# Kernel optimization log

Measured on AMD Instinct MI355X. Metric: run time of the kernel, lower is better.

Reference implementation:

```python
import jax, jax.numpy as jnp
import numpy as np

EMB = 1024
HEADS = 16
HEAD_DIM = EMB // HEADS
B, T = 2, 2048
LN_EPS = 1e-5  # torch nn.LayerNorm default


def _layernorm(x, g, b):
    # LayerNorm over last dim (head_dim), elementwise affine
    mu = jnp.mean(x, axis=-1, keepdims=True)
    var = jnp.mean(jnp.square(x - mu), axis=-1, keepdims=True)
    return (x - mu) * jax.lax.rsqrt(var + LN_EPS) * g + b


def setup_inputs() -> dict:
    key = jax.random.key(0)
    ks = jax.random.split(key, 6)
    sc = 1.0 / np.sqrt(EMB)  # keep linear outputs O(1)
    return {
        "x": jax.random.normal(ks[0], (B, T, EMB), dtype=jnp.float32),
        "Wk": jax.random.normal(ks[1], (EMB, EMB), dtype=jnp.float32) * sc,
        "Wq": jax.random.normal(ks[2], (EMB, EMB), dtype=jnp.float32) * sc,
        "Wv": jax.random.normal(ks[3], (EMB, EMB), dtype=jnp.float32) * sc,
        "Wu": jax.random.normal(ks[4], (EMB, EMB), dtype=jnp.float32) * sc,
        "bu": jnp.zeros((EMB,), dtype=jnp.float32),
        "kln_g": jnp.ones((HEAD_DIM,), dtype=jnp.float32),
        "kln_b": jnp.zeros((HEAD_DIM,), dtype=jnp.float32),
        "qln_g": jnp.ones((HEAD_DIM,), dtype=jnp.float32),
        "qln_b": jnp.zeros((HEAD_DIM,), dtype=jnp.float32),
    }


def reference(x, Wk, Wq, Wv, Wu, bu, kln_g, kln_b, qln_g, qln_b):
    b, t, e = x.shape
    h, s = HEADS, HEAD_DIM
    # torch Linear (no bias): y = x @ W.T
    keys = (x @ Wk.T).reshape(b, t, h, s)
    queries = (x @ Wq.T).reshape(b, t, h, s)
    values = (x @ Wv.T).reshape(b, t, h, s)
    # per-head LayerNorm (kqnorm=True)
    keys = _layernorm(keys, kln_g, kln_b)
    queries = _layernorm(queries, qln_g, qln_b)
    # NOTE: module scales by emb**(-1/4) on each side (net 1/sqrt(emb), not head dim)
    inv4 = e ** (-0.25)
    queries = queries * inv4
    keys = keys * inv4
    # scores: [b, h, t, t]
    dot = jnp.einsum('bqhs,bkhs->bhqk', queries, keys)
    # causal mask: positions k > q set to -inf (mask_diagonal=False -> diag kept)
    causal = jnp.tril(jnp.ones((t, t), dtype=bool))
    dot = jnp.where(causal, dot, -jnp.inf)
    attn = jax.nn.softmax(dot, axis=-1)
    out = jnp.einsum('bhqk,bkhs->bqhs', attn, values).reshape(b, t, h * s)
    return out @ Wu.T + bu
```

## Files before the change

### kernel.cpp

```cpp
#include <hip/hip_runtime.h>
#include <math.h>

#define EMB 1024
#define NHEADS 16
#define HDIM 64
#define BATCH 2
#define SEQ 2048
#define MROWS (BATCH*SEQ)
#define LN_EPS 1e-5f
#define GK 1024
#define GN 1024

typedef __attribute__((ext_vector_type(8))) short bf16x8;
typedef __attribute__((ext_vector_type(4))) short s16x4;
typedef __attribute__((ext_vector_type(4))) float f32x4;
typedef __attribute__((ext_vector_type(16))) float f32x16;
typedef __attribute__((ext_vector_type(4))) int int4v;

__device__ __forceinline__ short f2bf(float f) {
    union { float f; unsigned u; } v; v.f = f;
    unsigned r = v.u + 0x7FFFu + ((v.u >> 16) & 1u);
    return (short)(r >> 16);
}
__device__ __forceinline__ float bf2f(short s) {
    union { unsigned u; float f; } v; v.u = ((unsigned)(unsigned short)s) << 16;
    return v.f;
}
__device__ __forceinline__ unsigned pk2(short a, short b) {
    return (unsigned)(unsigned short)a | ((unsigned)(unsigned short)b << 16);
}
__device__ __forceinline__ float fexp2(float x) {
    return __builtin_amdgcn_exp2f(x);
}

__device__ __forceinline__ void gload16(const short* g, short* l) {
    __builtin_amdgcn_global_load_lds(
        (const __attribute__((address_space(1))) unsigned*)g,
        (__attribute__((address_space(3))) unsigned*)l, 16, 0, 0);
}

#define MFMA32(a, b, c) __builtin_amdgcn_mfma_f32_32x32x16_bf16(a, b, c, 0, 0, 0)

#define SRC_G(r, c)  ((((c) - ((r) >> 1)) & 3) * 8)
#define RD_G(r, l4)  ((((l4) + ((r) >> 1)) & 3) * 8)

__global__ __launch_bounds__(256)
void cvt_all(const float* __restrict__ X, short* __restrict__ XH,
             const float* __restrict__ W0, const float* __restrict__ W1,
             const float* __restrict__ W2, const float* __restrict__ W3,
             short* __restrict__ WH)
{
    const int zy = blockIdx.y;
    if (zy == 0) {
        const size_t i = (size_t)blockIdx.x * 1024 + threadIdx.x * 4;
        const float4 v = *(const float4*)&X[i];
        s16x4 h;
        h[0] = f2bf(v.x); h[1] = f2bf(v.y);
        h[2] = f2bf(v.z); h[3] = f2bf(v.w);
        *(s16x4*)&XH[i] = h;
    } else {
        const int z = zy - 1;
        if (blockIdx.x >= 1024) return;
        const float* W = (z == 0) ? W0 : (z == 1) ? W1 : (z == 2) ? W2 : W3;
        const size_t i = (size_t)blockIdx.x * 1024 + threadIdx.x * 4;
        const float4 v = *(const float4*)&W[i];
        s16x4 h;
        h[0] = f2bf(v.x); h[1] = f2bf(v.y);
        h[2] = f2bf(v.z); h[3] = f2bf(v.w);
        *(s16x4*)&WH[((size_t)z << 20) + i] = h;
    }
}

__global__ __launch_bounds__(256, 3)
void gemm_kqv(const short* __restrict__ Xh, const short* __restrict__ W4h,
              const float* __restrict__ kg, const float* __restrict__ kb,
              const float* __restrict__ qg, const float* __restrict__ qb,
              float scaleK, float scaleQ,
              short* __restrict__ KhP, short* __restrict__ QhP,
              short* __restrict__ VTh)
{
    __shared__ short AhS[3][128][32], BhS[3][128][32];

    const int t   = threadIdx.x;
    const int ln  = t & 63, wv = t >> 6;
    const int l15 = ln & 15, l4 = ln >> 4;
    const int m0  = blockIdx.y * 128;
    const int n0  = blockIdx.x * 128;
    const int z   = blockIdx.z;
    const int wr  = (wv >> 1) * 64, wc = (wv & 1) * 64;

    const short* Bh = W4h + ((size_t)z << 20);

    const short* gplane = (wv < 2) ? Xh : Bh;
    const int    grow0  = (wv < 2) ? m0 : n0;
    short* lbase = (wv < 2) ? &AhS[0][0][0] : &BhS[0][0][0];
    const int s0 = (wv & 1) ? 4 : 0;

    f32x4 acc[4][4];
    #pragma unroll
    for (int i = 0; i < 4; ++i)
        #pragma unroll
        for (int j = 0; j < 4; ++j) acc[i][j] = (f32x4){0.f, 0.f, 0.f, 0.f};

    #pragma unroll
    for (int s = 0; s < 4; ++s) {
        const int chunk = (s0 + s) * 64 + ln;
        const int r = chunk >> 2, c = chunk & 3;
        gload16(gplane + (size_t)(grow0 + r) * GK + SRC_G(r, c),
                lbase + (s0 + s) * 512);
    }
    #pragma unroll
    for (int s = 0; s < 4; ++s) {
        const int chunk = (s0 + s) * 64 + ln;
        const int r = chunk >> 2, c = chunk & 3;
        gload16(gplane + (size_t)(grow0 + r) * GK + 32 + SRC_G(r, c),
                lbase + 4096 + (s0 + s) * 512);
    }
    asm volatile("s_waitcnt vmcnt(4)" ::: "memory");
    __builtin_amdgcn_s_barrier();

    int cur = 0;
    for (int i = 0; i < 32; ++i) {
        const int cur2 = (cur == 0) ? 2 : cur - 1;
        if (i + 2 < 32) {
            short* lp = lbase + cur2 * 4096;
            const int kof = (i + 2) * 32;
            #pragma unroll
            for (int s = 0; s < 4; ++s) {
                const int chunk = (s0 + s) * 64 + ln;
                const int r = chunk >> 2, c = chunk & 3;
                gload16(gplane + (size_t)(grow0 + r) * GK + kof + SRC_G(r, c),
                        lp + (s0 + s) * 512);
            }
        }

        bf16x8 ah[4], bh[4];
        #pragma unroll
        for (int f = 0; f < 4; ++f) {
            const int ra = wr + f * 16 + l15;
            const int rb = wc + f * 16 + l15;
            ah[f] = *(const bf16x8*)&AhS[cur][ra][RD_G(ra, l4)];
            bh[f] = *(const bf16x8*)&BhS[cur][rb][RD_G(rb, l4)];
        }
        #pragma unroll
        for (int i2 = 0; i2 < 4; ++i2)
            #pragma unroll
            for (int j = 0; j < 4; ++j)
                acc[i2][j] = __builtin_amdgcn_mfma_f32_16x16x32_bf16(ah[i2], bh[j], acc[i2][j], 0, 0, 0);

        if (i + 2 < 32) {
            asm volatile("s_waitcnt vmcnt(4)" ::: "memory");
        } else if (i + 1 < 32) {
            asm volatile("s_waitcnt vmcnt(0)" ::: "memory");
        }
        __builtin_amdgcn_s_barrier();
        cur = (cur == 2) ? 0 : cur + 1;
    }

    if (z < 2) {
        const float* gamma = (z == 0) ? kg : qg;
        const float* beta  = (z == 0) ? kb : qb;
        short* OutH = (z == 0) ? KhP : QhP;
        const float scl = (z == 0) ? scaleK : scaleQ;
        const int n_head = (n0 + wc) >> 6;
        float g4[4], b4[4];
        #pragma unroll
        for (int f = 0; f < 4; ++f) {
            g4[f] = gamma[f * 16 + l15];
            b4[f] = beta [f * 16 + l15];
        }
        #pragma unroll
        for (int i = 0; i < 4; ++i)
            #pragma unroll
            for (int j = 0; j < 4; ++j) {
                const float v0 = acc[i][0][j], v1 = acc[i][1][j];
                const float v2 = acc[i][2][j], v3 = acc[i][3][j];
                float s1 = v0 + v1 + v2 + v3;
                float s2 = v0*v0 + v1*v1 + v2*v2 + v3*v3;
                s1 += __shfl_xor(s1, 1); s2 += __shfl_xor(s2, 1);
                s1 += __shfl_xor(s1, 2); s2 += __shfl_xor(s2, 2);
                s1 += __shfl_xor(s1, 4); s2 += __shfl_xor(s2, 4);
                s1 += __shfl_xor(s1, 8); s2 += __shfl_xor(s2, 8);
                const float mu  = s1 * (1.f / 64.f);
                const float var = s2 * (1.f / 64.f) - mu * mu;
                const float rs  = rsqrtf(var + LN_EPS);
                const int m = m0 + wr + i * 16 + l4 * 4 + j;
                const size_t orow =
                    ((size_t)((m >> 11) * NHEADS + n_head) * SEQ + (m & (SEQ - 1))) * HDIM;
                #pragma unroll
                for (int f = 0; f < 4; ++f) {
                    const float y = ((acc[i][f][j] - mu) * rs * g4[f] + b4[f]) * scl;
                    OutH[orow + f * 16 + l15] = f2bf(y);
                }
            }
    } else {
        #pragma unroll
        for (int i = 0; i < 4; ++i)
            #pragma unroll
            for (int f = 0; f < 4; ++f) {
                s16x4 h4;
                #pragma unroll
                for (int j = 0; j < 4; ++j) h4[j] = f2bf(acc[i][f][j]);
                const int n  = n0 + wc + f * 16 + l15;
                const int hh = n >> 6, dd = n & 63;
                const int mb = m0 + wr + i * 16 + l4 * 4;
                const size_t oa =
                    (((size_t)((mb >> 11) * NHEADS + hh)) * HDIM + dd) * SEQ + (mb & (SEQ - 1));
                *(s16x4*)&VTh[oa] = h4;
            }
    }
}

__global__ __launch_bounds__(256, 2)
void gemm_out(const short* __restrict__ Ah, const short* __restrict__ Bh,
              const float* __restrict__ bias, float* __restrict__ OutF)
{
    __shared__ short AhS[2][64][32], BhS[2][128][32];

    const int t   = threadIdx.x;
    const int ln  = t & 63, wv = t >> 6;
    const int l15 = ln & 15, l4 = ln >> 4;
    const int m0  = blockIdx.y * 64;
    const int n0  = blockIdx.x * 128;
    const int wr  = (wv >> 1) * 32, wc = (wv & 1) * 64;

    const short* gplane = (wv == 0) ? Ah : Bh;
    const int    grow0  = (wv == 0) ? m0 : n0;
    const int    s0     = (wv == 2) ? 4 : 0;
    const int    nseg   = (wv < 3) ? 4 : 0;
    const int    bstep  = (wv == 0) ? 2048 : 4096;
    short* lbase = (wv == 0) ? &AhS[0][0][0] : &BhS[0][0][0];

    f32x4 acc[2][4];
    #pragma unroll
    for (int i = 0; i < 2; ++i)
        #pragma unroll
        for (int j = 0; j < 4; ++j) acc[i][j] = (f32x4){0.f, 0.f, 0.f, 0.f};

    for (int s = 0; s < nseg; ++s) {
        const int chunk = (s0 + s) * 64 + ln;
        const int r = chunk >> 2, c = chunk & 3;
        gload16(gplane + (size_t)(grow0 + r) * GK + SRC_G(r, c),
                lbase + (s0 + s) * 512);
    }
    __syncthreads();

    int cur = 0;
    for (int k0 = 0; k0 < GK; k0 += 32) {
        if (k0 + 32 < GK) {
            short* lp = lbase + (cur ^ 1) * bstep;
            for (int s = 0; s < nseg; ++s) {
                const int chunk = (s0 + s) * 64 + ln;
                const int r = chunk >> 2, c = chunk & 3;
                gload16(gplane + (size_t)(grow0 + r) * GK + k0 + 32 + SRC_G(r, c),
                        lp + (s0 + s) * 512);
            }
        }

        bf16x8 ah[2], bh[4];
        #pragma unroll
        for (int f = 0; f < 2; ++f) {
            const int ra = wr + f * 16 + l15;
            ah[f] = *(const bf16x8*)&AhS[cur][ra][RD_G(ra, l4)];
        }
        #pragma unroll
        for (int f = 0; f < 4; ++f) {
            const int rb = wc + f * 16 + l15;
            bh[f] = *(const bf16x8*)&BhS[cur][rb][RD_G(rb, l4)];
        }
        #pragma unroll
        for (int i = 0; i < 2; ++i)
            #pragma unroll
            for (int j = 0; j < 4; ++j)
                acc[i][j] = __builtin_amdgcn_mfma_f32_16x16x32_bf16(ah[i], bh[j], acc[i][j], 0, 0, 0);

        __syncthreads();
        cur ^= 1;
    }

    float b4[4];
    #pragma unroll
    for (int f = 0; f < 4; ++f) b4[f] = bias[n0 + wc + f * 16 + l15];
    #pragma unroll
    for (int i = 0; i < 2; ++i)
        #pragma unroll
        for (int j = 0; j < 4; ++j) {
            const int m = m0 + wr + i * 16 + l4 * 4 + j;
            const size_t row = (size_t)m * GN + n0 + wc;
            #pragma unroll
            for (int f = 0; f < 4; ++f)
                OutF[row + f * 16 + l15] = acc[i][f][j] + b4[f];
        }
}

__global__ __launch_bounds__(256, 2)
void attn_mfma(const short* __restrict__ Qh, const short* __restrict__ Kh,
               const short* __restrict__ Vh, short* __restrict__ Oh)
{
    __shared__ short KhS[64][64];
    __shared__ short VhS[64][64];

    const int t    = threadIdx.x;
    const int lane = t & 63, wv = t >> 6;
    const int l31  = lane & 31, hb = lane >> 5;
    const int bh   = blockIdx.y;
    const int bb   = bh >> 4, hh = bh & 15;
    const int qt   = bb ? (int)blockIdx.x
                        : (int)gridDim.x - 1 - (int)blockIdx.x;
    const int q0   = qt * 128;
    const int wq0  = wv * 32;

    const size_t kpan = (size_t)bh * SEQ * HDIM;
    const size_t vpan = (size_t)bh * HDIM * SEQ;

    const int sr0  = t >> 3, sr1 = 32 + (t >> 3);
    const int scg  = t & 7;
    const int soff = scg * 8;
    const int lc0  = (scg ^ (sr0 & 7)) * 8;
    const int lc1  = (scg ^ (sr1 & 7)) * 8;

    bf16x8 qfh[4];
    {
        const size_t qrow = kpan + (size_t)(q0 + wq0 + l31) * HDIM;
        #pragma unroll
        for (int ds = 0; ds < 4; ++ds)
            qfh[ds] = *(const bf16x8*)&Qh[qrow + ds * 16 + hb * 8];
    }

    f32x16 oacc0 = (f32x16)(0.0f), oacc1 = (f32x16)(0.0f);
    float m_run = -1e30f, l_run = 0.f;

    const int NT = 2 * qt + 2;

    int4v pKh0, pKh1, pVh0, pVh1;
    {
        pKh0 = *(const int4v*)&Kh[kpan + (size_t)sr0 * HDIM + soff];
        pKh1 = *(const int4v*)&Kh[kpan + (size_t)sr1 * HDIM + soff];
        pVh0 = *(const int4v*)&Vh[vpan + (size_t)sr0 * SEQ + soff];
        pVh1 = *(const int4v*)&Vh[vpan + (size_t)sr1 * SEQ + soff];
    }

    for (int kt = 0; kt < NT; ++kt) {
        const int k0 = kt * 64;

        __syncthreads();

        *(int4v*)&KhS[sr0][lc0] = pKh0;  *(int4v*)&KhS[sr1][lc1] = pKh1;
        *(int4v*)&VhS[sr0][lc0] = pVh0;  *(int4v*)&VhS[sr1][lc1] = pVh1;

        if (kt + 1 < NT) {
            const int kn = k0 + 64;
            pKh0 = *(const int4v*)&Kh[kpan + (size_t)(kn + sr0) * HDIM + soff];
            pKh1 = *(const int4v*)&Kh[kpan + (size_t)(kn + sr1) * HDIM + soff];
            pVh0 = *(const int4v*)&Vh[vpan + (size_t)sr0 * SEQ + kn + soff];
            pVh1 = *(const int4v*)&Vh[vpan + (size_t)sr1 * SEQ + kn + soff];
        }
        __syncthreads();

        if (k0 > q0 + wq0 + 31) continue;

        f32x16 s0 = (f32x16)(0.0f), s1 = (f32x16)(0.0f);
        #pragma unroll
        for (int ds = 0; ds < 4; ++ds) {
            const int g = ((ds * 2 + hb) ^ (l31 & 7)) * 8;
            const bf16x8 kh0 = *(const bf16x8*)&KhS[l31][g];
            const bf16x8 kh1 = *(const bf16x8*)&KhS[32 + l31][g];
            s0 = MFMA32(kh0, qfh[ds], s0);
            s1 = MFMA32(kh1, qfh[ds], s1);
        }

        if (k0 + 63 > q0 + wq0) {
            const int qg = q0 + wq0 + l31;
            #pragma unroll
            for (int reg = 0; reg < 16; ++reg) {
                const int kk = k0 + (reg & 3) + 8 * (reg >> 2) + 4 * hb;
                if (kk > qg)      s0[reg] = -1e30f;
                if (kk + 32 > qg) s1[reg] = -1e30f;
            }
        }

        {
            float mx = -1e30f;
            #pragma unroll
            for (int reg = 0; reg < 16; ++reg)
                mx = fmaxf(mx, fmaxf(s0[reg], s1[reg]));
            mx = fmaxf(mx, __shfl_xor(mx, 32));
            const float mnew = fmaxf(m_run, mx);
            const float scf  = fexp2(m_run - mnew);
            m_run = mnew;
            float ls = 0.f;
            #pragma unroll
            for (int reg = 0; reg < 16; ++reg) {
                const float p0 = fexp2(s0[reg] - mnew);
                const float p1 = fexp2(s1[reg] - mnew);
                s0[reg] = p0; s1[reg] = p1;
                ls += p0 + p1;
            }
            ls += __shfl_xor(ls, 32);
            l_run = l_run * scf + ls;
            #pragma unroll
            for (int reg = 0; reg < 16; ++reg) {
                oacc0[reg] *= scf;
                oacc1[reg] *= scf;
            }
        }

        #pragma unroll
        for (int ks = 0; ks < 4; ++ks) {
            short h8[8];
            #pragma unroll
            for (int a = 0; a < 8; ++a) {
                const float p = (ks >= 2) ? s1[(ks & 1) * 8 + a]
                                          : s0[(ks & 1) * 8 + a];
                h8[a] = f2bf(p);
            }
            const unsigned hA0 = pk2(h8[0], h8[1]), hA1 = pk2(h8[2], h8[3]);
            const unsigned hB0 = pk2(h8[4], h8[5]), hB1 = pk2(h8[6], h8[7]);
            const unsigned hr0 = (unsigned)__shfl_xor((int)(hb ? hA0 : hB0), 32);
            const unsigned hr1 = (unsigned)__shfl_xor((int)(hb ? hA1 : hB1), 32);
            const int4v wih = (int4v){(int)(hb ? hr0 : hA0), (int)(hb ? hr1 : hA1),
                                      (int)(hb ? hB0 : hr0), (int)(hb ? hB1 : hr1)};
            const bf16x8 pfh = __builtin_bit_cast(bf16x8, wih);

            const int gv = ((ks * 2 + hb) ^ (l31 & 7)) * 8;
            const bf16x8 vh0 = *(const bf16x8*)&VhS[l31][gv];
            const bf16x8 vh1 = *(const bf16x8*)&VhS[32 + l31][gv];
            oacc0 = MFMA32(vh0, pfh, oacc0);
            oacc1 = MFMA32(vh1, pfh, oacc1);
        }
    }

    const float inv = 1.f / l_run;
    const int q = q0 + wq0 + l31;
    const size_t row = ((size_t)(bb * SEQ + q)) * EMB + hh * HDIM;
    #pragma unroll
    for (int db = 0; db < 2; ++db)
        #pragma unroll
        for (int b = 0; b < 4; ++b) {
            s16x4 h4;
            #pragma unroll
            for (int a = 0; a < 4; ++a)
                h4[a] = f2bf((db ? oacc1[4 * b + a] : oacc0[4 * b + a]) * inv);
            const int d0 = db * 32 + 8 * b + 4 * hb;
            *(s16x4*)&Oh[row + d0] = h4;
        }
}

extern "C" void kernel_launch(void* const* d_in, const int* in_sizes, int n_in,
                              void* d_out, int out_size, void* d_ws, size_t ws_size,
                              hipStream_t stream)
{
    const float* x  = (const float*)d_in[0];
    const float* Wk = (const float*)d_in[1];
    const float* Wq = (const float*)d_in[2];
    const float* Wv = (const float*)d_in[3];
    const float* Wu = (const float*)d_in[4];
    const float* bu = (const float*)d_in[5];
    const float* kg = (const float*)d_in[6];
    const float* kb = (const float*)d_in[7];
    const float* qg = (const float*)d_in[8];
    const float* qb = (const float*)d_in[9];
    float* out = (float*)d_out;

    char* w = (char*)d_ws;
    short* XhP = (short*)(w);
    short* KhP = (short*)(w + (8u  << 20));
    short* QhP = (short*)(w + (16u << 20));
    short* W4h = (short*)(w + (24u << 20));
    short* VTh = (short*)d_out;

    const float inv4 = 0.17677669529663687f;
    const float l2e  = 1.4426950408889634f;

    cvt_all<<<dim3(4096, 5), 256, 0, stream>>>(x, XhP, Wk, Wq, Wv, Wu, W4h);

    gemm_kqv<<<dim3(GN / 128, MROWS / 128, 3), 256, 0, stream>>>(
        XhP, W4h, kg, kb, qg, qb, inv4, inv4 * l2e,
        KhP, QhP, VTh);

    attn_mfma<<<dim3(SEQ / 128, BATCH * NHEADS), 256, 0, stream>>>(
        QhP, KhP, VTh, XhP);

    gemm_out<<<dim3(GN / 128, MROWS / 64), 256, 0, stream>>>(
        XhP, W4h + (3u << 20), bu, out);
}
```

Before: 121.6 us.

## Stage two K/V tiles per barrier round and skip redundant softmax rescales

```diff
diff --git a/kernel.cpp b/kernel.cpp
--- a/kernel.cpp
+++ b/kernel.cpp
@@ -297,8 +297,8 @@
 void attn_mfma(const short* __restrict__ Qh, const short* __restrict__ Kh,
                const short* __restrict__ Vh, short* __restrict__ Oh)
 {
-    __shared__ short KhS[64][64];
-    __shared__ short VhS[64][64];
+    __shared__ short KhS[2][64][64];
+    __shared__ short VhS[2][64][64];
 
     const int t    = threadIdx.x;
     const int lane = t & 63, wv = t >> 6;
@@ -317,7 +317,6 @@
     const int scg  = t & 7;
     const int soff = scg * 8;
     const int lc0  = (scg ^ (sr0 & 7)) * 8;
-    const int lc1  = (scg ^ (sr1 & 7)) * 8;
 
     bf16x8 qfh[4];
     {
@@ -330,103 +329,121 @@
     f32x16 oacc0 = (f32x16)(0.0f), oacc1 = (f32x16)(0.0f);
     float m_run = -1e30f, l_run = 0.f;
 
-    const int NT = 2 * qt + 2;
-
-    int4v pKh0, pKh1, pVh0, pVh1;
-    {
-        pKh0 = *(const int4v*)&Kh[kpan + (size_t)sr0 * HDIM + soff];
-        pKh1 = *(const int4v*)&Kh[kpan + (size_t)sr1 * HDIM + soff];
-        pVh0 = *(const int4v*)&Vh[vpan + (size_t)sr0 * SEQ + soff];
-        pVh1 = *(const int4v*)&Vh[vpan + (size_t)sr1 * SEQ + soff];
-    }
-
-    for (int kt = 0; kt < NT; ++kt) {
-        const int k0 = kt * 64;
+    const int NR = qt + 1;
+
+    int4v pK[2][2], pV[2][2];
+    #pragma unroll
+    for (int h = 0; h < 2; ++h) {
+        const int kb0 = h * 64;
+        pK[h][0] = *(const int4v*)&Kh[kpan + (size_t)(kb0 + sr0) * HDIM + soff];
+        pK[h][1] = *(const int4v*)&Kh[kpan + (size_t)(kb0 + sr1) * HDIM + soff];
+        pV[h][0] = *(const int4v*)&Vh[vpan + (size_t)sr0 * SEQ + kb0 + soff];
+        pV[h][1] = *(const int4v*)&Vh[vpan + (size_t)sr1 * SEQ + kb0 + soff];
+    }
+
+    for (int rr = 0; rr < NR; ++rr) {
+        const int k0 = rr * 128;
 
         __syncthreads();
 
-        *(int4v*)&KhS[sr0][lc0] = pKh0;  *(int4v*)&KhS[sr1][lc1] = pKh1;
-        *(int4v*)&VhS[sr0][lc0] = pVh0;  *(int4v*)&VhS[sr1][lc1] = pVh1;
-
-        if (kt + 1 < NT) {
-            const int kn = k0 + 64;
-            pKh0 = *(const int4v*)&Kh[kpan + (size_t)(kn + sr0) * HDIM + soff];
-            pKh1 = *(const int4v*)&Kh[kpan + (size_t)(kn + sr1) * HDIM + soff];
-            pVh0 = *(const int4v*)&Vh[vpan + (size_t)sr0 * SEQ + kn + soff];
-            pVh1 = *(const int4v*)&Vh[vpan + (size_t)sr1 * SEQ + kn + soff];
+        #pragma unroll
+        for (int h = 0; h < 2; ++h) {
+            *(int4v*)&KhS[h][sr0][lc0] = pK[h][0];
+            *(int4v*)&KhS[h][sr1][lc0] = pK[h][1];
+            *(int4v*)&VhS[h][sr0][lc0] = pV[h][0];
+            *(int4v*)&VhS[h][sr1][lc0] = pV[h][1];
+        }
+
+        if (rr + 1 < NR) {
+            const int kn = k0 + 128;
+            #pragma unroll
+            for (int h = 0; h < 2; ++h) {
+                const int kb0 = kn + h * 64;
+                pK[h][0] = *(const int4v*)&Kh[kpan + (size_t)(kb0 + sr0) * HDIM + soff];
+                pK[h][1] = *(const int4v*)&Kh[kpan + (size_t)(kb0 + sr1) * HDIM + soff];
+                pV[h][0] = *(const int4v*)&Vh[vpan + (size_t)sr0 * SEQ + kb0 + soff];
+                pV[h][1] = *(const int4v*)&Vh[vpan + (size_t)sr1 * SEQ + kb0 + soff];
+            }
         }
         __syncthreads();
 
-        if (k0 > q0 + wq0 + 31) continue;
-
-        f32x16 s0 = (f32x16)(0.0f), s1 = (f32x16)(0.0f);
-        #pragma unroll
-        for (int ds = 0; ds < 4; ++ds) {
-            const int g = ((ds * 2 + hb) ^ (l31 & 7)) * 8;
-            const bf16x8 kh0 = *(const bf16x8*)&KhS[l31][g];
-            const bf16x8 kh1 = *(const bf16x8*)&KhS[32 + l31][g];
-            s0 = MFMA32(kh0, qfh[ds], s0);
-            s1 = MFMA32(kh1, qfh[ds], s1);
-        }
-
-        if (k0 + 63 > q0 + wq0) {
-            const int qg = q0 + wq0 + l31;
-            #pragma unroll
-            for (int reg = 0; reg < 16; ++reg) {
-                const int kk = k0 + (reg & 3) + 8 * (reg >> 2) + 4 * hb;
-                if (kk > qg)      s0[reg] = -1e30f;
-                if (kk + 32 > qg) s1[reg] = -1e30f;
-            }
-        }
-
-        {
-            float mx = -1e30f;
-            #pragma unroll
-            for (int reg = 0; reg < 16; ++reg)
-                mx = fmaxf(mx, fmaxf(s0[reg], s1[reg]));
-            mx = fmaxf(mx, __shfl_xor(mx, 32));
-            const float mnew = fmaxf(m_run, mx);
-            const float scf  = fexp2(m_run - mnew);
-            m_run = mnew;
-            float ls = 0.f;
-            #pragma unroll
-            for (int reg = 0; reg < 16; ++reg) {
-                const float p0 = fexp2(s0[reg] - mnew);
-                const float p1 = fexp2(s1[reg] - mnew);
-                s0[reg] = p0; s1[reg] = p1;
-                ls += p0 + p1;
-            }
-            ls += __shfl_xor(ls, 32);
-            l_run = l_run * scf + ls;
-            #pragma unroll
-            for (int reg = 0; reg < 16; ++reg) {
-                oacc0[reg] *= scf;
-                oacc1[reg] *= scf;
-            }
-        }
-
-        #pragma unroll
-        for (int ks = 0; ks < 4; ++ks) {
-            short h8[8];
-            #pragma unroll
-            for (int a = 0; a < 8; ++a) {
-                const float p = (ks >= 2) ? s1[(ks & 1) * 8 + a]
-                                          : s0[(ks & 1) * 8 + a];
-                h8[a] = f2bf(p);
-            }
-            const unsigned hA0 = pk2(h8[0], h8[1]), hA1 = pk2(h8[2], h8[3]);
-            const unsigned hB0 = pk2(h8[4], h8[5]), hB1 = pk2(h8[6], h8[7]);
-            const unsigned hr0 = (unsigned)__shfl_xor((int)(hb ? hA0 : hB0), 32);
-            const unsigned hr1 = (unsigned)__shfl_xor((int)(hb ? hA1 : hB1), 32);
-            const int4v wih = (int4v){(int)(hb ? hr0 : hA0), (int)(hb ? hr1 : hA1),
-                                      (int)(hb ? hB0 : hr0), (int)(hb ? hB1 : hr1)};
-            const bf16x8 pfh = __builtin_bit_cast(bf16x8, wih);
-
-            const int gv = ((ks * 2 + hb) ^ (l31 & 7)) * 8;
-            const bf16x8 vh0 = *(const bf16x8*)&VhS[l31][gv];
-            const bf16x8 vh1 = *(const bf16x8*)&VhS[32 + l31][gv];
-            oacc0 = MFMA32(vh0, pfh, oacc0);
-            oacc1 = MFMA32(vh1, pfh, oacc1);
+        #pragma unroll
+        for (int half = 0; half < 2; ++half) {
+            const int kk0 = k0 + half * 64;
+            if (kk0 > q0 + wq0 + 31) continue;
+
+            f32x16 s0 = (f32x16)(0.0f), s1 = (f32x16)(0.0f);
+            #pragma unroll
+            for (int ds = 0; ds < 4; ++ds) {
+                const int g = ((ds * 2 + hb) ^ (l31 & 7)) * 8;
+                const bf16x8 kh0 = *(const bf16x8*)&KhS[half][l31][g];
+                const bf16x8 kh1 = *(const bf16x8*)&KhS[half][32 + l31][g];
+                s0 = MFMA32(kh0, qfh[ds], s0);
+                s1 = MFMA32(kh1, qfh[ds], s1);
+            }
+
+            if (kk0 + 63 > q0 + wq0) {
+                const int qg = q0 + wq0 + l31;
+                #pragma unroll
+                for (int reg = 0; reg < 16; ++reg) {
+                    const int kk = kk0 + (reg & 3) + 8 * (reg >> 2) + 4 * hb;
+                    if (kk > qg)      s0[reg] = -1e30f;
+                    if (kk + 32 > qg) s1[reg] = -1e30f;
+                }
+            }
+
+            {
+                float mx = -1e30f;
+                #pragma unroll
+                for (int reg = 0; reg < 16; ++reg)
+                    mx = fmaxf(mx, fmaxf(s0[reg], s1[reg]));
+                mx = fmaxf(mx, __shfl_xor(mx, 32));
+                if (__any(mx > m_run)) {
+                    const float mnew = fmaxf(m_run, mx);
+                    const float scf  = fexp2(m_run - mnew);
+                    m_run = mnew;
+                    l_run *= scf;
+                    #pragma unroll
+                    for (int reg = 0; reg < 16; ++reg) {
+                        oacc0[reg] *= scf;
+                        oacc1[reg] *= scf;
+                    }
+                }
+                float ls = 0.f;
+                #pragma unroll
+                for (int reg = 0; reg < 16; ++reg) {
+                    const float p0 = fexp2(s0[reg] - m_run);
+                    const float p1 = fexp2(s1[reg] - m_run);
+                    s0[reg] = p0; s1[reg] = p1;
+                    ls += p0 + p1;
+                }
+                ls += __shfl_xor(ls, 32);
+                l_run += ls;
+            }
+
+            #pragma unroll
+            for (int ks = 0; ks < 4; ++ks) {
+                short h8[8];
+                #pragma unroll
+                for (int a = 0; a < 8; ++a) {
+                    const float p = (ks >= 2) ? s1[(ks & 1) * 8 + a]
+                                              : s0[(ks & 1) * 8 + a];
+                    h8[a] = f2bf(p);
+                }
+                const unsigned hA0 = pk2(h8[0], h8[1]), hA1 = pk2(h8[2], h8[3]);
+                const unsigned hB0 = pk2(h8[4], h8[5]), hB1 = pk2(h8[6], h8[7]);
+                const unsigned hr0 = (unsigned)__shfl_xor((int)(hb ? hA0 : hB0), 32);
+                const unsigned hr1 = (unsigned)__shfl_xor((int)(hb ? hA1 : hB1), 32);
+                const int4v wih = (int4v){(int)(hb ? hr0 : hA0), (int)(hb ? hr1 : hA1),
+                                          (int)(hb ? hB0 : hr0), (int)(hb ? hB1 : hr1)};
+                const bf16x8 pfh = __builtin_bit_cast(bf16x8, wih);
+
+                const int gv = ((ks * 2 + hb) ^ (l31 & 7)) * 8;
+                const bf16x8 vh0 = *(const bf16x8*)&VhS[half][l31][gv];
+                const bf16x8 vh1 = *(const bf16x8*)&VhS[half][32 + l31][gv];
+                oacc0 = MFMA32(vh0, pfh, oacc0);
+                oacc1 = MFMA32(vh1, pfh, oacc1);
+            }
         }
     }
 
```

Measured after the change: 117.5 us. -3.4%, faster.
